# Kernel optimization log

Measured on AMD Instinct MI355X. Metric: run time of the kernel, lower is better.

## Reference

```python
import jax, jax.numpy as jnp
import numpy as np

# Irreps structure: (multiplicity, component dim 2l+1) for 64x0e + 32x1o + 16x2e
MULTS = (64, 32, 16)
DIMS = (1, 3, 5)
N_NODES = 65536
NUM_TYPES = 64


def setup_inputs() -> dict:
    key = jax.random.key(0)
    k_x, k_idx, k0, k1, k2 = jax.random.split(key, 5)
    dim = sum(m * d for m, d in zip(MULTS, DIMS))  # 240
    x = jax.random.normal(k_x, (N_NODES, dim), dtype=jnp.float32)
    idx = jax.random.randint(k_idx, (N_NODES,), 0, NUM_TYPES)
    W0 = jax.random.normal(k0, (NUM_TYPES, 64, 64), dtype=jnp.float32)
    W1 = jax.random.normal(k1, (NUM_TYPES, 32, 32), dtype=jnp.float32)
    W2 = jax.random.normal(k2, (NUM_TYPES, 16, 16), dtype=jnp.float32)
    return {"x": x, "W0": W0, "W1": W1, "W2": W2, "idx": idx}


def reference(x, W0, W1, W2, idx):
    """Indexed e3nn-style linear: per-node index gathers a weight set; each
    irrep block mixes multiplicity channels (shared across the 2l+1 components)
    with e3nn path normalization 1/sqrt(m_in)."""
    n = x.shape[0]
    outs = []
    off = 0
    for W, m, d in zip((W0, W1, W2), MULTS, DIMS):
        blk = x[:, off:off + m * d].reshape(n, m, d)  # [N, m_in, 2l+1]
        off += m * d
        Wn = W[idx]  # gather per-node weights: [N, m_in, m_out]
        scale = np.float32(1.0 / np.sqrt(m))
        out = jnp.einsum('nio,nid->nod', Wn, blk) * scale  # [N, m_out, 2l+1]
        outs.append(out.reshape(n, m * d))
    return jnp.concatenate(outs, axis=-1)
```

## Files before the change

kernel.cpp:

```cpp
#include <hip/hip_runtime.h>

typedef __attribute__((ext_vector_type(8))) short short8;
typedef __attribute__((ext_vector_type(4))) float floatx4;
typedef __attribute__((ext_vector_type(4))) unsigned uintx4;

#define NTYPES    64
#define WT_STRIDE 5632
#define WROWS     16
#define CPAD      16

__device__ __forceinline__ unsigned short f2bf(float f) {
    union { float f; unsigned u; } v; v.f = f;
    unsigned u = v.u;
    u += 0x7FFFu + ((u >> 16) & 1u);
    return (unsigned short)(u >> 16);
}

__device__ __forceinline__ unsigned pk2(float lo, float hi) {
    unsigned r;
    asm("v_cvt_pk_bf16_f32 %0, %1, %2" : "=v"(r) : "v"(lo), "v"(hi));
    return r;
}

__global__ __launch_bounds__(256) void wt_kernel(const float* __restrict__ W0,
                                                 const float* __restrict__ W1,
                                                 const float* __restrict__ W2,
                                                 const int* __restrict__ idx,
                                                 unsigned short* __restrict__ wt,
                                                 int* __restrict__ bh, int n) {
    __shared__ float ws0[4096];
    __shared__ float ws1[1024];
    __shared__ float ws2[256];
    __shared__ int hc[NTYPES];
    const int t = blockIdx.x, tid = threadIdx.x;
    if (tid < NTYPES) hc[tid] = 0;
    const float4* s0 = (const float4*)(W0 + (size_t)t * 4096);
#pragma unroll
    for (int j = 0; j < 4; ++j) ((float4*)ws0)[j * 256 + tid] = s0[j * 256 + tid];
    ((float4*)ws1)[tid] = ((const float4*)(W1 + (size_t)t * 1024))[tid];
    if (tid < 64) ((float4*)ws2)[tid] = ((const float4*)(W2 + (size_t)t * 256))[tid];
    __syncthreads();
    const int per = (n + NTYPES - 1) / NTYPES;
    for (int e = tid; e < per; e += 256) {
        int g = t * per + e;
        if (g < n) atomicAdd(&hc[idx[g]], 1);
    }
    unsigned short* dst = wt + (size_t)t * WT_STRIDE;
    for (int e = tid; e < 4096; e += 256) {
        int f = e >> 9, rem = e & 511, rr = rem >> 5, k2 = rem & 31;
        int i = (f & 1) * 32 + k2, o = (f >> 1) * 16 + rr;
        dst[e] = f2bf(ws0[i * 64 + o] * 0.125f);
    }
    for (int e = tid; e < 1024; e += 256) {
        int h = e >> 9, rem = e & 511, rr = rem >> 5, k = rem & 31;
        dst[4096 + e] = f2bf(ws1[k * 32 + h * 16 + rr] * 0.17677669529663687f);
    }
    for (int e = tid; e < 512; e += 256) {
        int rr = e >> 5, k = e & 31;
        dst[5120 + e] = (k < 16) ? f2bf(ws2[k * 16 + rr] * 0.25f) : (unsigned short)0;
    }
    __syncthreads();
    if (tid < NTYPES) bh[t * NTYPES + tid] = hc[tid];
}

__global__ __launch_bounds__(64) void base_kernel(const int* __restrict__ bh,
                                                  int* __restrict__ gcur) {
    const int t = threadIdx.x;
    int v = 0;
#pragma unroll
    for (int b = 0; b < NTYPES; ++b) v += bh[b * NTYPES + t];
    int s = v;
#pragma unroll
    for (int o = 1; o < 64; o <<= 1) {
        int u = __shfl_up(s, o);
        if (t >= o) s += u;
    }
    gcur[t * CPAD] = s - v;
}

__global__ __launch_bounds__(256) void scatter_kernel(const int* __restrict__ idx,
                                                      int* __restrict__ gcur,
                                                      int* __restrict__ psort, int n) {
    __shared__ int c[NTYPES], off[NTYPES], cur[NTYPES];
    const int tid = threadIdx.x, g = blockIdx.x * 256 + tid;
    if (tid < NTYPES) { c[tid] = 0; cur[tid] = 0; }
    __syncthreads();
    int ty = -1;
    if (g < n) { ty = idx[g]; atomicAdd(&c[ty], 1); }
    __syncthreads();
    if (tid < NTYPES && c[tid]) off[tid] = atomicAdd(&gcur[tid * CPAD], c[tid]);
    __syncthreads();
    if (g < n) {
        int rk = atomicAdd(&cur[ty], 1);
        psort[off[ty] + rk] = g | (ty << 24);
    }
}

#define LOAD_FRAGS(WB) do {                                         \
    const unsigned short* _wp = (WB) + r * 32 + q4 * 8;             \
    wa0 = *(const short8*)(_wp);                                    \
    wa1 = *(const short8*)(_wp + 512);                              \
    wa2 = *(const short8*)(_wp + 1024);                             \
    wa3 = *(const short8*)(_wp + 1536);                             \
    wa4 = *(const short8*)(_wp + 2048);                             \
    wa5 = *(const short8*)(_wp + 2560);                             \
    wa6 = *(const short8*)(_wp + 3072);                             \
    wa7 = *(const short8*)(_wp + 3584);                             \
    wc0 = *(const short8*)(_wp + 4096);                             \
    wc1 = *(const short8*)(_wp + 4608);                             \
    wc2 = *(const short8*)(_wp + 5120);                             \
} while (0)

__global__ __launch_bounds__(256, 3) void main_kernel(
    const float* __restrict__ x,
    const int* __restrict__ psort,
    const unsigned short* __restrict__ wt,
    float* __restrict__ out, int n)
{
    const int tid = threadIdx.x, wv = tid >> 6, ln = tid & 63;
    const int w = blockIdx.x * 4 + wv;
    const int nbase = w * WROWS;
    if (nbase >= n) return;
    const int nv = min(WROWS, n - nbase);

    int pl = 0;
    if (ln < WROWS && (nbase + ln) < n) pl = psort[nbase + ln];

    const int r = ln & 15, q4 = ln >> 4;
    const int prow = __shfl(pl, min(r, nv - 1));
    const int node = prow & 0xFFFFFF;
    const float* xp = x + (size_t)node * 240;

    int ti  = __shfl(pl, r) >> 24;
    int tim = __shfl(pl, (r > 0) ? (r - 1) : 0) >> 24;
    bool bnd = (r == 0) || (ti != tim);
    unsigned m = (unsigned)(__ballot(bnd) & 0xFFFFull);
    const int ty0 = __shfl(pl, 0) >> 24;

    float4 f0a = *(const float4*)(xp + q4 * 8);
    float4 f0b = *(const float4*)(xp + q4 * 8 + 4);
    float4 f0c = *(const float4*)(xp + 32 + q4 * 8);
    float4 f0d = *(const float4*)(xp + 32 + q4 * 8 + 4);
    const float4* xg = (const float4*)(xp + 64 + q4 * 24);
    float4 g0 = xg[0], g1 = xg[1], g2 = xg[2], g3 = xg[3], g4 = xg[4], g5 = xg[5];
    const float4* xh = (const float4*)(xp + 160 + (q4 & 1) * 40);
    float4 h0 = xh[0], h1 = xh[1], h2 = xh[2], h3 = xh[3], h4 = xh[4];
    float4 h5 = xh[5], h6 = xh[6], h7 = xh[7], h8 = xh[8], h9 = xh[9];
    short8 wa0, wa1, wa2, wa3, wa4, wa5, wa6, wa7, wc0, wc1, wc2;
    LOAD_FRAGS(wt + (size_t)ty0 * WT_STRIDE);
    __builtin_amdgcn_sched_barrier(0);

    union frag { short8 s; uintx4 u; };

    frag bx0, bx1;
    bx0.u = uintx4{pk2(f0a.x, f0a.y), pk2(f0a.z, f0a.w),
                   pk2(f0b.x, f0b.y), pk2(f0b.z, f0b.w)};
    bx1.u = uintx4{pk2(f0c.x, f0c.y), pk2(f0c.z, f0c.w),
                   pk2(f0d.x, f0d.y), pk2(f0d.z, f0d.w)};
    const float G[24] = {g0.x, g0.y, g0.z, g0.w, g1.x, g1.y, g1.z, g1.w,
                         g2.x, g2.y, g2.z, g2.w, g3.x, g3.y, g3.z, g3.w,
                         g4.x, g4.y, g4.z, g4.w, g5.x, g5.y, g5.z, g5.w};
    frag b1d[3];
#pragma unroll
    for (int d = 0; d < 3; ++d)
        b1d[d].u = uintx4{pk2(G[d], G[3 + d]), pk2(G[6 + d], G[9 + d]),
                          pk2(G[12 + d], G[15 + d]), pk2(G[18 + d], G[21 + d])};
    const float H[40] = {h0.x, h0.y, h0.z, h0.w, h1.x, h1.y, h1.z, h1.w,
                         h2.x, h2.y, h2.z, h2.w, h3.x, h3.y, h3.z, h3.w,
                         h4.x, h4.y, h4.z, h4.w, h5.x, h5.y, h5.z, h5.w,
                         h6.x, h6.y, h6.z, h6.w, h7.x, h7.y, h7.z, h7.w,
                         h8.x, h8.y, h8.z, h8.w, h9.x, h9.y, h9.z, h9.w};
    frag b2d[5];
#pragma unroll
    for (int d = 0; d < 5; ++d)
        b2d[d].u = uintx4{pk2(H[d], H[5 + d]), pk2(H[10 + d], H[15 + d]),
                          pk2(H[20 + d], H[25 + d]), pk2(H[30 + d], H[35 + d])};

    const bool vrow = (r < nv);
    float* op = out + (size_t)node * 240;

    while (true) {
        const int slo = __builtin_ctz(m);
        const unsigned m2 = m & (m - 1u);
        const int shi = m2 ? __builtin_ctz(m2) : nv;
        const bool vst = vrow && (r >= slo) && (r < shi);

        {
            floatx4 ac;
            ac = floatx4{0.f, 0.f, 0.f, 0.f};
            ac = __builtin_amdgcn_mfma_f32_16x16x32_bf16(wa0, bx0.s, ac, 0, 0, 0);
            ac = __builtin_amdgcn_mfma_f32_16x16x32_bf16(wa1, bx1.s, ac, 0, 0, 0);
            if (vst) *(floatx4*)(op + q4 * 4) = ac;
            ac = floatx4{0.f, 0.f, 0.f, 0.f};
            ac = __builtin_amdgcn_mfma_f32_16x16x32_bf16(wa2, bx0.s, ac, 0, 0, 0);
            ac = __builtin_amdgcn_mfma_f32_16x16x32_bf16(wa3, bx1.s, ac, 0, 0, 0);
            if (vst) *(floatx4*)(op + 16 + q4 * 4) = ac;
            ac = floatx4{0.f, 0.f, 0.f, 0.f};
            ac = __builtin_amdgcn_mfma_f32_16x16x32_bf16(wa4, bx0.s, ac, 0, 0, 0);
            ac = __builtin_amdgcn_mfma_f32_16x16x32_bf16(wa5, bx1.s, ac, 0, 0, 0);
            if (vst) *(floatx4*)(op + 32 + q4 * 4) = ac;
            ac = floatx4{0.f, 0.f, 0.f, 0.f};
            ac = __builtin_amdgcn_mfma_f32_16x16x32_bf16(wa6, bx0.s, ac, 0, 0, 0);
            ac = __builtin_amdgcn_mfma_f32_16x16x32_bf16(wa7, bx1.s, ac, 0, 0, 0);
            if (vst) *(floatx4*)(op + 48 + q4 * 4) = ac;
        }

        {
            floatx4 a1[2][3];
#pragma unroll
            for (int d = 0; d < 3; ++d) {
                floatx4 z = {0.f, 0.f, 0.f, 0.f};
                a1[0][d] = __builtin_amdgcn_mfma_f32_16x16x32_bf16(wc0, b1d[d].s, z, 0, 0, 0);
                a1[1][d] = __builtin_amdgcn_mfma_f32_16x16x32_bf16(wc1, b1d[d].s, z, 0, 0, 0);
            }
            if (vst) {
#pragma unroll
                for (int h = 0; h < 2; ++h) {
                    float* o1 = op + 64 + (h * 16 + q4 * 4) * 3;
                    floatx4 v0 = {a1[h][0][0], a1[h][1][0], a1[h][2][0], a1[h][0][1]};
                    floatx4 v1 = {a1[h][1][1], a1[h][2][1], a1[h][0][2], a1[h][1][2]};
                    floatx4 v2 = {a1[h][2][2], a1[h][0][3], a1[h][1][3], a1[h][2][3]};
                    *(floatx4*)(o1)     = v0;
                    *(floatx4*)(o1 + 4) = v1;
                    *(floatx4*)(o1 + 8) = v2;
                }
            }
        }

        {
            floatx4 a2[5];
#pragma unroll
            for (int d = 0; d < 5; ++d) {
                floatx4 z = {0.f, 0.f, 0.f, 0.f};
                a2[d] = __builtin_amdgcn_mfma_f32_16x16x32_bf16(wc2, b2d[d].s, z, 0, 0, 0);
            }
            if (vst) {
                float* o2 = op + 160 + q4 * 20;
                floatx4 v0 = {a2[0][0], a2[1][0], a2[2][0], a2[3][0]};
                floatx4 v1 = {a2[4][0], a2[0][1], a2[1][1], a2[2][1]};
                floatx4 v2 = {a2[3][1], a2[4][1], a2[0][2], a2[1][2]};
                floatx4 v3 = {a2[2][2], a2[3][2], a2[4][2], a2[0][3]};
                floatx4 v4 = {a2[1][3], a2[2][3], a2[3][3], a2[4][3]};
                *(floatx4*)(o2)      = v0;
                *(floatx4*)(o2 + 4)  = v1;
                *(floatx4*)(o2 + 8)  = v2;
                *(floatx4*)(o2 + 12) = v3;
                *(floatx4*)(o2 + 16) = v4;
            }
        }

        m = m2;
        if (!m) break;
        const int tyn = __shfl(pl, __builtin_ctz(m)) >> 24;
        LOAD_FRAGS(wt + (size_t)tyn * WT_STRIDE);
    }
}

extern "C" void kernel_launch(void* const* d_in, const int* in_sizes, int n_in,
                              void* d_out, int out_size, void* d_ws, size_t ws_size,
                              hipStream_t stream) {
    const float* x  = (const float*)d_in[0];
    const float* W0 = (const float*)d_in[1];
    const float* W1 = (const float*)d_in[2];
    const float* W2 = (const float*)d_in[3];
    const int*   idx = (const int*)d_in[4];
    float* out = (float*)d_out;
    const int n = in_sizes[4];
    const int nb = (n + 255) / 256;

    char* ws = (char*)d_ws;
    unsigned short* wt = (unsigned short*)ws;
    size_t off = (size_t)NTYPES * WT_STRIDE * 2;
    int* psort = (int*)(ws + off); off += (size_t)n * 4;
    int* bh    = (int*)(ws + off); off += (size_t)NTYPES * NTYPES * 4;
    int* gcur  = (int*)(ws + off);

    wt_kernel     <<<NTYPES, 256, 0, stream>>>(W0, W1, W2, idx, wt, bh, n);
    base_kernel   <<<1, 64, 0, stream>>>(bh, gcur);
    scatter_kernel<<<nb, 256, 0, stream>>>(idx, gcur, psort, n);
    main_kernel   <<<(n + 4 * WROWS - 1) / (4 * WROWS), 256, 0, stream>>>(x, psort, wt, out, n);
}
```

Baseline: 149.9 us.

## Stage gathered x rows through LDS via global_load_lds with single-wave blocks

Each wave now gathers its 16 node rows of x into shared memory using direct global-to-LDS 16-byte loads laid out contiguously across lanes, then reads the fragments from LDS. The old code had each lane issue scattered float4 loads from global memory. Blocks shrink to one wave of 64 threads, each using 16KB of LDS. The aim is better-coalesced gather traffic, at the cost of an LDS round trip, a full vmcnt wait before compute, and an occupancy limit set by LDS.

```diff
diff --git a/kernel.cpp b/kernel.cpp
--- a/kernel.cpp
+++ b/kernel.cpp
@@ -8,6 +8,7 @@
 #define WT_STRIDE 5632
 #define WROWS     16
 #define CPAD      16
+#define RSTRIDE   976
 
 __device__ __forceinline__ unsigned short f2bf(float f) {
     union { float f; unsigned u; } v; v.f = f;
@@ -111,15 +112,15 @@
     wc2 = *(const short8*)(_wp + 5120);                             \
 } while (0)
 
-__global__ __launch_bounds__(256, 3) void main_kernel(
+__global__ __launch_bounds__(64) void main_kernel(
     const float* __restrict__ x,
     const int* __restrict__ psort,
     const unsigned short* __restrict__ wt,
     float* __restrict__ out, int n)
 {
-    const int tid = threadIdx.x, wv = tid >> 6, ln = tid & 63;
-    const int w = blockIdx.x * 4 + wv;
-    const int nbase = w * WROWS;
+    __shared__ __align__(16) unsigned char xl[16384];
+    const int ln = threadIdx.x;
+    const int nbase = blockIdx.x * WROWS;
     if (nbase >= n) return;
     const int nv = min(WROWS, n - nbase);
 
@@ -127,9 +128,6 @@
     if (ln < WROWS && (nbase + ln) < n) pl = psort[nbase + ln];
 
     const int r = ln & 15, q4 = ln >> 4;
-    const int prow = __shfl(pl, min(r, nv - 1));
-    const int node = prow & 0xFFFFFF;
-    const float* xp = x + (size_t)node * 240;
 
     int ti  = __shfl(pl, r) >> 24;
     int tim = __shfl(pl, (r > 0) ? (r - 1) : 0) >> 24;
@@ -137,18 +135,35 @@
     unsigned m = (unsigned)(__ballot(bnd) & 0xFFFFull);
     const int ty0 = __shfl(pl, 0) >> 24;
 
-    float4 f0a = *(const float4*)(xp + q4 * 8);
-    float4 f0b = *(const float4*)(xp + q4 * 8 + 4);
-    float4 f0c = *(const float4*)(xp + 32 + q4 * 8);
-    float4 f0d = *(const float4*)(xp + 32 + q4 * 8 + 4);
-    const float4* xg = (const float4*)(xp + 64 + q4 * 24);
-    float4 g0 = xg[0], g1 = xg[1], g2 = xg[2], g3 = xg[3], g4 = xg[4], g5 = xg[5];
-    const float4* xh = (const float4*)(xp + 160 + (q4 & 1) * 40);
-    float4 h0 = xh[0], h1 = xh[1], h2 = xh[2], h3 = xh[3], h4 = xh[4];
-    float4 h5 = xh[5], h6 = xh[6], h7 = xh[7], h8 = xh[8], h9 = xh[9];
+#pragma unroll
+    for (int k = 0; k < 16; ++k) {
+        int L = k * 1024 + ln * 16;
+        int row = (int)(((unsigned)(L >> 4) * 1075u) >> 16);
+        int col = L - row * RSTRIDE;
+        int node = __shfl(pl, min(row, 15)) & 0xFFFFFF;
+        int colc = min(col, 944);
+        const float* src = x + (size_t)node * 240 + (colc >> 2);
+        __builtin_amdgcn_global_load_lds(
+            (const __attribute__((address_space(1))) void*)src,
+            (__attribute__((address_space(3))) void*)(xl + k * 1024),
+            16, 0, 0);
+    }
+
     short8 wa0, wa1, wa2, wa3, wa4, wa5, wa6, wa7, wc0, wc1, wc2;
     LOAD_FRAGS(wt + (size_t)ty0 * WT_STRIDE);
+
+    asm volatile("s_waitcnt vmcnt(0)" ::: "memory");
     __builtin_amdgcn_sched_barrier(0);
+
+    const float4* xr = (const float4*)(xl + r * RSTRIDE);
+    float4 f0a = xr[q4 * 2],     f0b = xr[q4 * 2 + 1];
+    float4 f0c = xr[8 + q4 * 2], f0d = xr[9 + q4 * 2];
+    float4 g0 = xr[16 + q4 * 6],     g1 = xr[16 + q4 * 6 + 1], g2 = xr[16 + q4 * 6 + 2];
+    float4 g3 = xr[16 + q4 * 6 + 3], g4 = xr[16 + q4 * 6 + 4], g5 = xr[16 + q4 * 6 + 5];
+    const int hb = 40 + (q4 & 1) * 10;
+    float4 h0 = xr[hb],     h1 = xr[hb + 1], h2 = xr[hb + 2], h3 = xr[hb + 3];
+    float4 h4 = xr[hb + 4], h5 = xr[hb + 5], h6 = xr[hb + 6], h7 = xr[hb + 7];
+    float4 h8 = xr[hb + 8], h9 = xr[hb + 9];
 
     union frag { short8 s; uintx4 u; };
 
@@ -177,7 +192,8 @@
                           pk2(H[20 + d], H[25 + d]), pk2(H[30 + d], H[35 + d])};
 
     const bool vrow = (r < nv);
-    float* op = out + (size_t)node * 240;
+    const int node_r = __shfl(pl, min(r, nv - 1)) & 0xFFFFFF;
+    float* op = out + (size_t)node_r * 240;
 
     while (true) {
         const int slo = __builtin_ctz(m);
@@ -278,5 +294,5 @@
     wt_kernel     <<<NTYPES, 256, 0, stream>>>(W0, W1, W2, idx, wt, bh, n);
     base_kernel   <<<1, 64, 0, stream>>>(bh, gcur);
     scatter_kernel<<<nb, 256, 0, stream>>>(idx, gcur, psort, n);
-    main_kernel   <<<(n + 4 * WROWS - 1) / (4 * WROWS), 256, 0, stream>>>(x, psort, wt, out, n);
-}
+    main_kernel   <<<(n + WROWS - 1) / WROWS, 64, 0, stream>>>(x, psort, wt, out, n);
+}
```

Measured after the change: 143.6 us. -4.2%, faster.
